# Kernel tuning notes

Measured on AMD Instinct MI355X. Metric: run time of the kernel, lower is better.

Reference implementation:

```python
import jax, jax.numpy as jnp
import numpy as np

B, N, H, W = 4, 128, 512, 512
VOCAB, HIDDEN, EDIM = 30522, 768, 64


def setup_inputs() -> dict:
    key = jax.random.key(0)
    k1, k2, k3, k4, k5, k6, k7, k8 = jax.random.split(key, 8)
    img = jax.random.normal(k1, (B, 3, H, W), dtype=jnp.float32)
    input_ids = jax.random.randint(k2, (B, N), 1, VOCAB, dtype=jnp.int32)
    # Realistic word boxes: (x0, y0, x1, y1) in pixel coords, x0<x1, y0<y1.
    x0 = jax.random.uniform(k3, (B, N), dtype=jnp.float32) * (W - 48.0)
    y0 = jax.random.uniform(k4, (B, N), dtype=jnp.float32) * (H - 16.0)
    bw = jax.random.uniform(k5, (B, N), dtype=jnp.float32) * 40.0 + 4.0
    bh = jax.random.uniform(k6, (B, N), dtype=jnp.float32) * 12.0 + 3.0
    bbox = jnp.stack([x0, y0, x0 + bw, y0 + bh], axis=-1)  # [B,N,4]
    emb_weight = jax.random.normal(k7, (VOCAB, HIDDEN), dtype=jnp.float32) * 0.02
    proj_weight = jax.random.normal(k8, (EDIM, HIDDEN), dtype=jnp.float32) * (1.0 / np.sqrt(HIDDEN))
    return {"img": img, "bbox": bbox, "emb_weight": emb_weight,
            "proj_weight": proj_weight, "input_ids": input_ids, "stride": 1}


def reference(img, bbox, emb_weight, proj_weight, input_ids, stride):
    Bb, _, Hf, Wf = img.shape
    Hg, Wg = Hf // stride, Wf // stride
    Nw = input_ids.shape[1]

    # Round boxes to integer grid coords (matches bbox/stride -> round -> int).
    b = jnp.round(bbox / stride).astype(jnp.int32)
    w0, h0, w1, h1 = b[..., 0], b[..., 1], b[..., 2], b[..., 3]

    hi = jnp.arange(Hg, dtype=jnp.int32)
    wi = jnp.arange(Wg, dtype=jnp.int32)
    cov_h = (hi[None, None, :] >= h0[:, :, None]) & (hi[None, None, :] < h1[:, :, None])  # [B,N,H]
    cov_w = (wi[None, None, :] >= w0[:, :, None]) & (wi[None, None, :] < w1[:, :, None])  # [B,N,W]

    prio = jnp.arange(1, Nw + 1, dtype=jnp.int32)  # 0 reserved for background
    covered = cov_h[:, :, :, None] & cov_w[:, :, None, :]              # [B,N,H,W]
    winner = jnp.max(jnp.where(covered, prio[None, :, None, None], 0), axis=1)  # [B,H,W]

    # Map winning word index -> token id (0 for background, as torch.zeros init).
    ids_ext = jnp.concatenate([jnp.zeros((Bb, 1), input_ids.dtype), input_ids], axis=1)  # [B,N+1]
    grid_ids = ids_ext[jnp.arange(Bb)[:, None, None], winner]           # [B,H,W]

    # embedding lookup + bias-free linear proj, fused into one small table:
    # (E[idx] @ Wp^T) == (E @ Wp^T)[idx]
    table = jnp.einsum('vh,eh->ve', emb_weight, proj_weight)            # [VOCAB,EDIM]
    out = table[grid_ids]                                               # [B,H,W,EDIM]
    return jnp.transpose(out, (0, 3, 1, 2))                             # [B,EDIM,H,W]
```

## Files before the change

### kernel.cpp

```cpp
#include <hip/hip_runtime.h>

#define BB     4
#define NW     128
#define HG     512
#define WG     512
#define EDIM   64
#define HIDDEN 768

typedef float f4 __attribute__((ext_vector_type(4)));

__global__ __launch_bounds__(256) void fused_kernel(
    const float* __restrict__ bbox,
    const float* __restrict__ emb,
    const float* __restrict__ proj,
    const int*   __restrict__ ids,
    const int*   __restrict__ stride_p,
    float*       __restrict__ out)
{
    const int t = threadIdx.x;
    const int lin = ((blockIdx.x & 7) << 7) | (blockIdx.x >> 3);
    const int b  = lin >> 8;
    const int e0 = ((lin >> 3) & 31) * 2;
    const int ht = lin & 7;
    const int rlo = ht * 64, rhi = rlo + 64;

    __shared__ unsigned entx[NW];
    __shared__ unsigned enty[NW];
    __shared__ int      sid[NW];
    __shared__ float    col0[NW + 1];
    __shared__ float    col1[NW + 1];
    __shared__ unsigned char sublist[8][NW];
    __shared__ int      subcnt[8];
    __shared__ int      cnt;

    if (t == 0) cnt = 0;
    if (t < 8)  subcnt[t] = 0;
    __syncthreads();

    if (t < NW) {
        const float s = (float)stride_p[0];
        float4 bv = ((const float4*)bbox)[b * NW + t];
        int w0 = (int)rintf(bv.x / s), h0 = (int)rintf(bv.y / s);
        int w1 = (int)rintf(bv.z / s), h1 = (int)rintf(bv.w / s);
        if (h1 > rlo && h0 < rhi && w1 > w0 && h1 > h0) {
            int i = atomicAdd(&cnt, 1);
            entx[i] = (unsigned)w0 | ((unsigned)w1 << 10) | ((unsigned)(t + 1) << 20);
            enty[i] = (unsigned)h0 | ((unsigned)h1 << 16);
            sid[i]  = ids[b * NW + t];
        }
    }
    __syncthreads();

    const int nc = cnt;
    const int wv = t >> 6, l = t & 63;

    if (t < nc) {
        const unsigned ey = enty[t];
        const int h0 = (int)(ey & 0xFFFFu), h1 = (int)(ey >> 16);
        #pragma unroll
        for (int st = 0; st < 8; ++st) {
            const int srl = rlo + st * 8;
            if (h1 > srl && h0 < srl + 8) {
                int k = atomicAdd(&subcnt[st], 1);
                sublist[st][k] = (unsigned char)t;
            }
        }
    }

    const f4* prbase0 = (const f4*)(proj + (size_t)e0 * HIDDEN) + l * 3;
    const f4* prbase1 = (const f4*)(proj + (size_t)(e0 + 1) * HIDDEN) + l * 3;
    f4 q00 = prbase0[0], q01 = prbase0[1], q02 = prbase0[2];
    f4 q10 = prbase1[0], q11 = prbase1[1], q12 = prbase1[2];

    for (int j = wv; j <= nc; j += 4) {
        const int id   = (j == nc) ? 0 : sid[j];
        const int slot = (j == nc) ? 0 : (int)(entx[j] >> 20);
        const f4* er = (const f4*)(emb + (size_t)id * HIDDEN) + l * 3;
        f4 a0 = er[0], a1 = er[1], a2 = er[2];
        float v0 = a0.x*q00.x + a0.y*q00.y + a0.z*q00.z + a0.w*q00.w
                 + a1.x*q01.x + a1.y*q01.y + a1.z*q01.z + a1.w*q01.w
                 + a2.x*q02.x + a2.y*q02.y + a2.z*q02.z + a2.w*q02.w;
        float v1 = a0.x*q10.x + a0.y*q10.y + a0.z*q10.z + a0.w*q10.w
                 + a1.x*q11.x + a1.y*q11.y + a1.z*q11.z + a1.w*q11.w
                 + a2.x*q12.x + a2.y*q12.y + a2.z*q12.z + a2.w*q12.w;
        #pragma unroll
        for (int m = 1; m < 64; m <<= 1) {
            v0 += __shfl_xor(v0, m, 64);
            v1 += __shfl_xor(v1, m, 64);
        }
        if (l == 0) { col0[slot] = v0; col1[slot] = v1; }
    }
    __syncthreads();

    float* obase0 = out + ((size_t)(b * EDIM + e0)) * HG * WG;
    float* obase1 = obase0 + (size_t)HG * WG;
    const int p0 = 4 * l, p1 = 256 + 4 * l;

    const float bgs0 = col0[0], bgs1 = col1[0];
    const f4 bgv0 = {bgs0, bgs0, bgs0, bgs0};
    const f4 bgv1 = {bgs1, bgs1, bgs1, bgs1};

    for (int rr = 0; rr < 16; ++rr) {
        const int ro  = wv * 16 + rr;
        const int row = rlo + ro;
        const int st  = ro >> 3;
        const int ns  = subcnt[st];
        f4* orow0 = (f4*)(obase0 + (size_t)row * WG);
        f4* orow1 = (f4*)(obase1 + (size_t)row * WG);

        if (ns == 0) {
            orow0[l]      = bgv0;
            orow0[64 + l] = bgv0;
            orow1[l]      = bgv1;
            orow1[64 + l] = bgv1;
            continue;
        }

        int wn0 = 0, wn1 = 0, wn2 = 0, wn3 = 0;
        int wn4 = 0, wn5 = 0, wn6 = 0, wn7 = 0;
        for (int k = 0; k < ns; ++k) {
            const int i = sublist[st][k];
            const unsigned ey = enty[i];
            const int h0 = (int)(ey & 0xFFFFu), h1 = (int)(ey >> 16);
            if (row >= h0 && row < h1) {
                const unsigned ex = entx[i];
                const int w0 = (int)(ex & 1023u);
                const int w1 = (int)((ex >> 10) & 1023u);
                const int pr = (int)(ex >> 20);
                if (p0     >= w0 && p0     < w1 && pr > wn0) wn0 = pr;
                if (p0 + 1 >= w0 && p0 + 1 < w1 && pr > wn1) wn1 = pr;
                if (p0 + 2 >= w0 && p0 + 2 < w1 && pr > wn2) wn2 = pr;
                if (p0 + 3 >= w0 && p0 + 3 < w1 && pr > wn3) wn3 = pr;
                if (p1     >= w0 && p1     < w1 && pr > wn4) wn4 = pr;
                if (p1 + 1 >= w0 && p1 + 1 < w1 && pr > wn5) wn5 = pr;
                if (p1 + 2 >= w0 && p1 + 2 < w1 && pr > wn6) wn6 = pr;
                if (p1 + 3 >= w0 && p1 + 3 < w1 && pr > wn7) wn7 = pr;
            }
        }
        f4 u0, u1, w0v, w1v;
        u0.x  = col0[wn0]; u0.y  = col0[wn1]; u0.z  = col0[wn2]; u0.w  = col0[wn3];
        u1.x  = col0[wn4]; u1.y  = col0[wn5]; u1.z  = col0[wn6]; u1.w  = col0[wn7];
        w0v.x = col1[wn0]; w0v.y = col1[wn1]; w0v.z = col1[wn2]; w0v.w = col1[wn3];
        w1v.x = col1[wn4]; w1v.y = col1[wn5]; w1v.z = col1[wn6]; w1v.w = col1[wn7];
        orow0[l]      = u0;
        orow0[64 + l] = u1;
        orow1[l]      = w0v;
        orow1[64 + l] = w1v;
    }
}

extern "C" void kernel_launch(void* const* d_in, const int* in_sizes, int n_in,
                              void* d_out, int out_size, void* d_ws, size_t ws_size,
                              hipStream_t stream)
{
    const float* bbox = (const float*)d_in[1];
    const float* emb  = (const float*)d_in[2];
    const float* proj = (const float*)d_in[3];
    const int*   ids  = (const int*)d_in[4];
    const int*   strd = (const int*)d_in[5];

    float* out = (float*)d_out;

    fused_kernel<<<1024, 256, 0, stream>>>(bbox, emb, proj, ids, strd, out);
}
```

Before: 62.90 us.

## Precompute per-word projected embeddings in a prep kernel before painting

Adds a prep kernel that computes, for each batch and word slot (plus background), the 64 projected embedding values via a tiled shared-memory dot product. The result goes into a transposed workspace table. The paint kernel then just loads its two columns from that table instead of redoing 768-long dot products with wave reductions in every block. This removes redundant projection work that was repeated across the 8 row-tile blocks per (batch, edim pair), at the cost of an extra kernel launch and a dependency on workspace memory.

```diff
diff --git a/kernel.cpp b/kernel.cpp
--- a/kernel.cpp
+++ b/kernel.cpp
@@ -6,15 +6,57 @@
 #define WG     512
 #define EDIM   64
 #define HIDDEN 768
+#define CTS    132
 
 typedef float f4 __attribute__((ext_vector_type(4)));
 
-__global__ __launch_bounds__(256) void fused_kernel(
-    const float* __restrict__ bbox,
+#define WS_CTABT  0
+
+__global__ __launch_bounds__(256) void prep_kernel(
     const float* __restrict__ emb,
     const float* __restrict__ proj,
     const int*   __restrict__ ids,
+    float*       __restrict__ ctabT)
+{
+    const int t  = threadIdx.x;
+    const int bx = blockIdx.x;
+
+    __shared__ float proj_s[64][68];
+    __shared__ float emb_s[4][68];
+
+    const int b = bx / 33, ng = bx % 33;
+    const int e = t & 63, r = t >> 6;
+    const int n = ng * 4 + r;
+    const bool valid = (n <= NW);
+    const int id = (!valid || n == 0) ? 0 : ids[b * NW + n - 1];
+    const float* erow = emb + (size_t)id * HIDDEN;
+
+    float acc = 0.f;
+    for (int kt = 0; kt < HIDDEN; kt += 64) {
+        if (e < 16)
+            *(f4*)&emb_s[r][e * 4] = ((const f4*)(erow + kt))[e];
+        #pragma unroll
+        for (int q = t; q < 1024; q += 256) {
+            const int pr = q >> 4, pc = q & 15;
+            *(f4*)&proj_s[pr][pc * 4] =
+                ((const f4*)(proj + (size_t)pr * HIDDEN + kt))[pc];
+        }
+        __syncthreads();
+        #pragma unroll
+        for (int k4 = 0; k4 < 16; ++k4) {
+            f4 a = *(const f4*)&emb_s[r][k4 * 4];
+            f4 p = *(const f4*)&proj_s[e][k4 * 4];
+            acc += a.x * p.x + a.y * p.y + a.z * p.z + a.w * p.w;
+        }
+        __syncthreads();
+    }
+    if (valid) ctabT[((size_t)(b * EDIM + e)) * CTS + n] = acc;
+}
+
+__global__ __launch_bounds__(256) void paint_kernel(
+    const float* __restrict__ bbox,
     const int*   __restrict__ stride_p,
+    const float* __restrict__ ctabT,
     float*       __restrict__ out)
 {
     const int t = threadIdx.x;
@@ -26,7 +68,6 @@
 
     __shared__ unsigned entx[NW];
     __shared__ unsigned enty[NW];
-    __shared__ int      sid[NW];
     __shared__ float    col0[NW + 1];
     __shared__ float    col1[NW + 1];
     __shared__ unsigned char sublist[8][NW];
@@ -46,7 +87,6 @@
             int i = atomicAdd(&cnt, 1);
             entx[i] = (unsigned)w0 | ((unsigned)w1 << 10) | ((unsigned)(t + 1) << 20);
             enty[i] = (unsigned)h0 | ((unsigned)h1 << 16);
-            sid[i]  = ids[b * NW + t];
         }
     }
     __syncthreads();
@@ -67,28 +107,12 @@
         }
     }
 
-    const f4* prbase0 = (const f4*)(proj + (size_t)e0 * HIDDEN) + l * 3;
-    const f4* prbase1 = (const f4*)(proj + (size_t)(e0 + 1) * HIDDEN) + l * 3;
-    f4 q00 = prbase0[0], q01 = prbase0[1], q02 = prbase0[2];
-    f4 q10 = prbase1[0], q11 = prbase1[1], q12 = prbase1[2];
-
-    for (int j = wv; j <= nc; j += 4) {
-        const int id   = (j == nc) ? 0 : sid[j];
+    for (int idx = t; idx < (nc + 1) * 2; idx += 256) {
+        const int j = idx >> 1, p = idx & 1;
         const int slot = (j == nc) ? 0 : (int)(entx[j] >> 20);
-        const f4* er = (const f4*)(emb + (size_t)id * HIDDEN) + l * 3;
-        f4 a0 = er[0], a1 = er[1], a2 = er[2];
-        float v0 = a0.x*q00.x + a0.y*q00.y + a0.z*q00.z + a0.w*q00.w
-                 + a1.x*q01.x + a1.y*q01.y + a1.z*q01.z + a1.w*q01.w
-                 + a2.x*q02.x + a2.y*q02.y + a2.z*q02.z + a2.w*q02.w;
-        float v1 = a0.x*q10.x + a0.y*q10.y + a0.z*q10.z + a0.w*q10.w
-                 + a1.x*q11.x + a1.y*q11.y + a1.z*q11.z + a1.w*q11.w
-                 + a2.x*q12.x + a2.y*q12.y + a2.z*q12.z + a2.w*q12.w;
-        #pragma unroll
-        for (int m = 1; m < 64; m <<= 1) {
-            v0 += __shfl_xor(v0, m, 64);
-            v1 += __shfl_xor(v1, m, 64);
-        }
-        if (l == 0) { col0[slot] = v0; col1[slot] = v1; }
+        const float v = ctabT[((size_t)(b * EDIM + e0 + p)) * CTS + slot];
+        if (p == 0) col0[slot] = v;
+        else        col1[slot] = v;
     }
     __syncthreads();
 
@@ -160,6 +184,10 @@
     const int*   strd = (const int*)d_in[5];
 
     float* out = (float*)d_out;
+    char*  ws  = (char*)d_ws;
+    float* ctabT = (float*)(ws + WS_CTABT);
 
-    fused_kernel<<<1024, 256, 0, stream>>>(bbox, emb, proj, ids, strd, out);
+    prep_kernel<<<132, 256, 0, stream>>>(emb, proj, ids, ctabT);
+
+    paint_kernel<<<1024, 256, 0, stream>>>(bbox, strd, ctabT, out);
 }
```

Result: slower. 85.34 us (+35.7%).
